# Kernel tuning notes

Measured on AMD Instinct MI355X. Metric: run time of the kernel, lower is better.

## Reference

```python
import jax, jax.numpy as jnp
import numpy as np

B, T, D = 16, 512, 512
T_OUT = 2560  # static cap on expanded length (mean total ~2048, +3 sigma << 2560)
MAX_DUR = 8.0


def setup_inputs() -> dict:
    key = jax.random.key(0)
    kx, kd = jax.random.split(key)
    x = jax.random.normal(kx, (B, T, D), dtype=jnp.float32)
    dur = jax.random.uniform(kd, (B, T), dtype=jnp.float32) * MAX_DUR
    return {"x": x, "dur": dur}


def reference(x, dur):
    # Rounded integer durations: (dur + 0.5).long() in torch == floor(dur + 0.5)
    d = jnp.floor(dur + 0.5).astype(jnp.int32)          # [B, T]
    ends = jnp.cumsum(d, axis=1)                         # [B, T] exclusive-end offsets
    pos = jnp.arange(T_OUT, dtype=jnp.int32)             # [T_OUT]
    # For output frame j, source phoneme = first t with ends[t] > j
    src = jax.vmap(lambda e: jnp.searchsorted(e, pos, side='right'))(ends)  # [B, T_OUT]
    src = jnp.minimum(src, x.shape[1] - 1)
    out = jnp.take_along_axis(x, src[:, :, None], axis=1)  # [B, T_OUT, D]
    valid = (pos[None, :] < ends[:, -1:]).astype(x.dtype)  # zero-pad beyond total length
    return out * valid[:, :, None]
```

## Files before the change

### kernel.cpp

```cpp
#include <hip/hip_runtime.h>
#include <math.h>


#define LR_B 16
#define LR_T 512
#define LR_D 512
#define LR_TOUT 2560
#define FRAMES_PER_BLOCK 16

__global__ __launch_bounds__(512) void lr_fused_kernel(
        const float* __restrict__ x,
        const float* __restrict__ dur,
        float* __restrict__ out) {
    const int b    = blockIdx.y;
    const int base = blockIdx.x * FRAMES_PER_BLOCK;
    const int tid  = threadIdx.x;
    const int lane = tid & 63;
    const int w    = tid >> 6;

    __shared__ int s[LR_T];
    __shared__ int wsum[8];

    int v = (int)floorf(dur[b * LR_T + tid] + 0.5f);
    #pragma unroll
    for (int off = 1; off < 64; off <<= 1) {
        int n = __shfl_up(v, off, 64);
        if (lane >= off) v += n;
    }
    if (lane == 63) wsum[w] = v;
    __syncthreads();
    if (tid < 8) {
        int t = wsum[tid];
        #pragma unroll
        for (int off = 1; off < 8; off <<= 1) {
            int n = __shfl_up(t, off, 8);
            if (tid >= off) t += n;
        }
        wsum[tid] = t;
    }
    __syncthreads();
    s[tid] = v + (w > 0 ? wsum[w - 1] : 0);
    __syncthreads();

    const int total = s[LR_T - 1];

    int r = -1;
    if (lane < 2) {
        const int j = base + 2 * w + lane;
        if (j < total) {
            int lo = 0, hi = LR_T;
            while (lo < hi) {
                int mid = (lo + hi) >> 1;
                if (s[mid] > j) hi = mid; else lo = mid + 1;
            }
            r = (lo < LR_T - 1) ? lo : (LR_T - 1);
        }
    }
    const int si0 = __shfl(r, 0, 64);
    const int si1 = __shfl(r, 1, 64);

    const size_t xb = (size_t)b * LR_T * LR_D;
    const size_t ob = (size_t)(b * LR_TOUT + base + 2 * w) * LR_D;

    float4 a0 = make_float4(0.f, 0.f, 0.f, 0.f), a1 = a0, b0 = a0, b1 = a0;
    if (si0 >= 0) {
        const float4* row = (const float4*)(x + xb + (size_t)si0 * LR_D);
        a0 = row[lane];
        a1 = row[lane + 64];
    }
    if (si1 >= 0) {
        const float4* row = (const float4*)(x + xb + (size_t)si1 * LR_D);
        b0 = row[lane];
        b1 = row[lane + 64];
    }
    float4* o0 = (float4*)(out + ob);
    float4* o1 = (float4*)(out + ob + LR_D);
    o0[lane]      = a0;
    o0[lane + 64] = a1;
    o1[lane]      = b0;
    o1[lane + 64] = b1;
}

extern "C" void kernel_launch(void* const* d_in, const int* in_sizes, int n_in,
                              void* d_out, int out_size, void* d_ws, size_t ws_size,
                              hipStream_t stream) {
    const float* x   = (const float*)d_in[0];
    const float* dur = (const float*)d_in[1];
    float* out = (float*)d_out;

    dim3 grid(LR_TOUT / FRAMES_PER_BLOCK, LR_B);
    lr_fused_kernel<<<grid, 512, 0, stream>>>(x, dur, out);
}
```

Baseline: 101.8 us.

## Double frames per block, drop a scan barrier, use nontemporal output stores

Each block now expands 32 output frames instead of 16, with every wave handling four rows in two unrolled pairs. This halves the number of blocks that redo the 512-element duration prefix scan. The second-level warp-sum scan and its barrier are replaced by each thread summing the preceding wave totals from shared memory. Output rows are written with nontemporal stores to avoid polluting cache with write-only data. Fewer blocks reduces parallelism, and nontemporal stores may behave differently on this hardware.

Result: slower. 106.3 us (+4.4%).

```diff
diff --git a/kernel.cpp b/kernel.cpp
--- a/kernel.cpp
+++ b/kernel.cpp
@@ -6,7 +6,9 @@
 #define LR_T 512
 #define LR_D 512
 #define LR_TOUT 2560
-#define FRAMES_PER_BLOCK 16
+#define FRAMES_PER_BLOCK 32
+
+typedef float f32x4 __attribute__((ext_vector_type(4)));
 
 __global__ __launch_bounds__(512) void lr_fused_kernel(
         const float* __restrict__ x,
@@ -29,56 +31,54 @@
     }
     if (lane == 63) wsum[w] = v;
     __syncthreads();
-    if (tid < 8) {
-        int t = wsum[tid];
-        #pragma unroll
-        for (int off = 1; off < 8; off <<= 1) {
-            int n = __shfl_up(t, off, 8);
-            if (tid >= off) t += n;
-        }
-        wsum[tid] = t;
-    }
-    __syncthreads();
-    s[tid] = v + (w > 0 ? wsum[w - 1] : 0);
+    int prefix = 0;
+    #pragma unroll
+    for (int i = 0; i < 7; ++i)
+        prefix += (i < w) ? wsum[i] : 0;
+    s[tid] = v + prefix;
     __syncthreads();
 
     const int total = s[LR_T - 1];
 
     int r = -1;
-    if (lane < 2) {
-        const int j = base + 2 * w + lane;
+    if (lane < 4) {
+        const int j = base + 4 * w + lane;
         if (j < total) {
             int lo = 0, hi = LR_T;
             while (lo < hi) {
-                int mid = (lo + hi) >> 1;
+                const int mid = (lo + hi) >> 1;
                 if (s[mid] > j) hi = mid; else lo = mid + 1;
             }
             r = (lo < LR_T - 1) ? lo : (LR_T - 1);
         }
     }
-    const int si0 = __shfl(r, 0, 64);
-    const int si1 = __shfl(r, 1, 64);
 
-    const size_t xb = (size_t)b * LR_T * LR_D;
-    const size_t ob = (size_t)(b * LR_TOUT + base + 2 * w) * LR_D;
+    const size_t xb    = (size_t)b * LR_T * LR_D;
+    const size_t obase = (size_t)(b * LR_TOUT + base + 4 * w) * LR_D;
 
-    float4 a0 = make_float4(0.f, 0.f, 0.f, 0.f), a1 = a0, b0 = a0, b1 = a0;
-    if (si0 >= 0) {
-        const float4* row = (const float4*)(x + xb + (size_t)si0 * LR_D);
-        a0 = row[lane];
-        a1 = row[lane + 64];
+    #pragma unroll
+    for (int p = 0; p < 2; ++p) {
+        const int sA = __shfl(r, 2 * p,     64);
+        const int sB = __shfl(r, 2 * p + 1, 64);
+
+        f32x4 a0 = {0.f, 0.f, 0.f, 0.f}, a1 = a0, c0 = a0, c1 = a0;
+        if (sA >= 0) {
+            const f32x4* row = (const f32x4*)(x + xb + (size_t)sA * LR_D);
+            a0 = row[lane];
+            a1 = row[lane + 64];
+        }
+        if (sB >= 0) {
+            const f32x4* row = (const f32x4*)(x + xb + (size_t)sB * LR_D);
+            c0 = row[lane];
+            c1 = row[lane + 64];
+        }
+        f32x4* oA = (f32x4*)(out + obase + (size_t)(2 * p)     * LR_D);
+        f32x4* oB = (f32x4*)(out + obase + (size_t)(2 * p + 1) * LR_D);
+        __builtin_nontemporal_store(a0, oA + lane);
+        __builtin_nontemporal_store(a1, oA + lane + 64);
+        __builtin_nontemporal_store(c0, oB + lane);
+        __builtin_nontemporal_store(c1, oB + lane + 64);
     }
-    if (si1 >= 0) {
-        const float4* row = (const float4*)(x + xb + (size_t)si1 * LR_D);
-        b0 = row[lane];
-        b1 = row[lane + 64];
-    }
-    float4* o0 = (float4*)(out + ob);
-    float4* o1 = (float4*)(out + ob + LR_D);
-    o0[lane]      = a0;
-    o0[lane + 64] = a1;
-    o1[lane]      = b0;
-    o1[lane + 64] = b1;
 }
 
 extern "C" void kernel_launch(void* const* d_in, const int* in_sizes, int n_in,
```
